# Optimization experiments

Measured on AMD Instinct MI355X. Metric: run time of the kernel, lower is better.

Reference implementation:

```python
import jax, jax.numpy as jnp
import numpy as np
from jax import lax

KS = 3
PAD = 1
N = KS * KS


def setup_inputs() -> dict:
    key = jax.random.key(0)
    k1, k2, k3, k4, k5, k6 = jax.random.split(key, 6)
    b, cin, cout, h, w = 4, 64, 64, 256, 256
    x = jax.random.normal(k1, (b, cin, h, w), jnp.float32)
    # offset-predicting conv: 2*N output channels, 3x3, pad 1
    p_conv_w = 0.1 * jax.random.normal(k2, (2 * N, cin, KS, KS), jnp.float32)
    p_conv_b = jnp.zeros((2 * N,), jnp.float32)
    # main conv applied to the k*k-expanded sampled map (no bias in original)
    conv_w = jax.random.normal(k3, (cout, cin, KS, KS), jnp.float32) / np.sqrt(cin * N)
    bn_gamma = 1.0 + 0.1 * jax.random.normal(k4, (cout,), jnp.float32)
    bn_beta = 0.1 * jax.random.normal(k5, (cout,), jnp.float32)
    return {"x": x, "p_conv_w": p_conv_w, "p_conv_b": p_conv_b,
            "conv_w": conv_w, "bn_gamma": bn_gamma, "bn_beta": bn_beta}


def _deform_conv(x, p_conv_w, p_conv_b, conv_w, bn_gamma, bn_beta):
    b, c, h, w = x.shape
    # offsets: (b, 2N, h, w) -> (b, h, w, 2N)
    offset = lax.conv_general_dilated(x, p_conv_w, (1, 1), ((PAD, PAD), (PAD, PAD)))
    offset = offset + p_conv_b[None, :, None, None]
    offset = jnp.transpose(offset, (0, 2, 3, 1))
    # zero-pad input; sampling coordinates live on the padded grid
    x_pad = jnp.pad(x, ((0, 0), (0, 0), (PAD, PAD), (PAD, PAD)))
    Hp, Wp = h + 2 * PAD, w + 2 * PAD
    # p = p_0 + p_n + offset  (x/y coords each of shape (b,h,w,N))
    r = jnp.arange(-(KS - 1) // 2, KS // 2 + 1, dtype=jnp.float32)  # [-1,0,1]
    pn_x, pn_y = jnp.meshgrid(r, r, indexing="ij")
    pn_x, pn_y = pn_x.reshape(-1), pn_y.reshape(-1)  # (N,)
    p0_x = jnp.arange(1, h + 1, dtype=jnp.float32)[:, None, None]  # (h,1,1)
    p0_y = jnp.arange(1, w + 1, dtype=jnp.float32)[None, :, None]  # (1,w,1)
    p_x = offset[..., :N] + p0_x + pn_x  # (b,h,w,N)
    p_y = offset[..., N:] + p0_y + pn_y
    # integer corner coords (detached / non-differentiable), clamped
    fx = jnp.floor(lax.stop_gradient(p_x))
    fy = jnp.floor(lax.stop_gradient(p_y))
    q_lt_x = jnp.clip(fx, 0, Hp - 1).astype(jnp.int32)
    q_lt_y = jnp.clip(fy, 0, Wp - 1).astype(jnp.int32)
    q_rb_x = jnp.clip(fx + 1, 0, Hp - 1).astype(jnp.int32)
    q_rb_y = jnp.clip(fy + 1, 0, Wp - 1).astype(jnp.int32)
    # clamped continuous coords (gradient flows to offsets)
    px = jnp.clip(p_x, 0, Hp - 1)
    py = jnp.clip(p_y, 0, Wp - 1)
    # bilinear weights
    ltx = q_lt_x.astype(px.dtype); lty = q_lt_y.astype(px.dtype)
    rbx = q_rb_x.astype(px.dtype); rby = q_rb_y.astype(px.dtype)
    g_lt = (1 + (ltx - px)) * (1 + (lty - py))
    g_rb = (1 - (rbx - px)) * (1 - (rby - py))
    g_lb = (1 + (ltx - px)) * (1 - (rby - py))
    g_rt = (1 - (rbx - px)) * (1 + (lty - py))
    x_flat = x_pad.reshape(b, c, Hp * Wp)

    def gather(qx, qy):
        idx = (qx * Wp + qy).reshape(b, 1, -1)  # (b,1,h*w*N)
        out = jnp.take_along_axis(x_flat, idx, axis=2)
        return out.reshape(b, c, h, w, N)

    x_off = (g_lt[:, None] * gather(q_lt_x, q_lt_y)
             + g_rb[:, None] * gather(q_rb_x, q_rb_y)
             + g_lb[:, None] * gather(q_lt_x, q_rb_y)
             + g_rt[:, None] * gather(q_rb_x, q_lt_y))  # (b,c,h,w,N)
    # conv (kernel=KS, stride=KS on k*k-expanded map) == contraction over (c,N)
    out = jnp.einsum("bchwn,ocn->bohw", x_off, conv_w.reshape(conv_w.shape[0], c, N))
    # BatchNorm2d (training-mode batch statistics) + LeakyReLU(0.1)
    mean = out.mean(axis=(0, 2, 3), keepdims=True)
    var = out.var(axis=(0, 2, 3), keepdims=True)
    y = (out - mean) * lax.rsqrt(var + 1e-5)
    y = y * bn_gamma[None, :, None, None] + bn_beta[None, :, None, None]
    return jnp.where(y > 0, y, 0.1 * y)


def reference(x, p_conv_w, p_conv_b, conv_w, bn_gamma, bn_beta):
    return _deform_conv(x, p_conv_w, p_conv_b, conv_w, bn_gamma, bn_beta)
```

## Files before the change

### kernel.cpp

```cpp
#include <hip/hip_runtime.h>
#include <math.h>

#define BB 4
#define CC 64
#define OCC 64
#define HH 256
#define WW 256
#define HP 258
#define WP 258
#define NPIX (BB * HH * WW)
#define CNT_F 262144.0f

typedef __attribute__((ext_vector_type(8))) __bf16 bf16x8;
typedef __attribute__((ext_vector_type(4))) float f32x4;

__global__ __launch_bounds__(256) void pad_transpose(const float* __restrict__ x,
                                                     __bf16* __restrict__ xt) {
    int blk = blockIdx.x;
    int xchunk = blk & 3;
    int y = (blk >> 2) & 255;
    int b = blk >> 10;
    int tid = threadIdx.x;
    __shared__ float tile[64][65];
    int x0 = xchunk * 64;
    int col = tid & 63;
    int crow = tid >> 6;
    const float* xp = x + ((size_t)b * CC) * HH * WW + (size_t)y * WW + x0;
#pragma unroll
    for (int i = 0; i < 16; ++i) {
        int c = crow + i * 4;
        tile[c][col] = xp[(size_t)c * HH * WW + col];
    }
    __syncthreads();
    __bf16* op = xt + (((size_t)b * HP + (y + 1)) * WP + (x0 + 1)) * CC;
#pragma unroll
    for (int i = 0; i < 16; ++i) {
        int xl = crow + i * 4;
        op[(size_t)xl * CC + col] = (__bf16)tile[col][xl];
    }
}

__global__ void zero_border(__bf16* __restrict__ xt) {
    int i = blockIdx.x * 256 + threadIdx.x;
    const int total = BB * 1028 * CC;
    if (i >= total) return;
    int c = i & 63;
    int p = (i >> 6) % 1028;
    int b = (i >> 6) / 1028;
    int yp, xp;
    if (p < 258)      { yp = 0;           xp = p; }
    else if (p < 516) { yp = 257;         xp = p - 258; }
    else if (p < 772) { yp = p - 516 + 1; xp = 0; }
    else              { yp = p - 772 + 1; xp = 257; }
    xt[(((size_t)b * HP + yp) * WP + xp) * CC + c] = (__bf16)0.0f;
}

__global__ void reorder_weights(const float* __restrict__ cw,
                                const float* __restrict__ pw,
                                __bf16* __restrict__ wtb,
                                __bf16* __restrict__ pwb) {
    int i = blockIdx.x * 256 + threadIdx.x;
    if (i < 36864) {
        int c = i & 63;
        int n = (i >> 6) % 9;
        int oc = i / 576;
        wtb[i] = (__bf16)cw[((size_t)oc * CC + c) * 9 + n];
    } else {
        int j = i - 36864;
        if (j >= 18432) return;
        int c = j & 63;
        int n = (j >> 6) % 9;
        int oc = j / 576;
        pwb[j] = (__bf16)(oc < 18 ? pw[((size_t)oc * CC + c) * 9 + n] : 0.0f);
    }
}

__global__ __launch_bounds__(256, 6) void offset_strip(const __bf16* __restrict__ xt,
                                                       const __bf16* __restrict__ pwb,
                                                       const float* __restrict__ pb,
                                                       float* __restrict__ off) {
    int phys = blockIdx.x;
    int blk = (phys & 7) * 1024 + (phys >> 3);
    int xq = blk & 7;
    int y  = (blk >> 3) & 255;
    int b  = blk >> 11;
    int x0 = xq * 32;
    int tid = threadIdx.x;
    int wave = tid >> 6, lane = tid & 63;

    __shared__ __attribute__((aligned(16))) __bf16 sS[3][34][72];
    __shared__ float sC[32][33];

    {
        const char* base = (const char*)xt + (size_t)b * HP * WP * CC * 2;
        for (int t = tid; t < 3264; t += 256) {
            int pos = t >> 5, cp = t & 31;
            int r = pos / 34, j = pos - r * 34;
            unsigned d = *(const unsigned*)(base
                + (size_t)((y + r) * WP + (x0 + j)) * (CC * 2) + cp * 4);
            *(unsigned*)&sS[r][j][cp * 2] = d;
        }
    }
    __syncthreads();

    {
        int mh = wave & 1, nh = wave >> 1;
        int m = lane & 15, q = lane >> 4;
        int p_a = mh * 16 + m;
        f32x4 acc = {0.0f, 0.0f, 0.0f, 0.0f};
        const __bf16* bp = pwb + (size_t)(nh * 16 + m) * 576 + q * 8;
#pragma unroll
        for (int n = 0; n < 9; ++n) {
            int dy = n / 3, dx = n - dy * 3;
            const __bf16* abase = &sS[dy][p_a + dx][q * 8];
#pragma unroll
            for (int h = 0; h < 2; ++h) {
                bf16x8 a  = *(const bf16x8*)(abase + h * 32);
                bf16x8 bv = *(const bf16x8*)(bp + n * 64 + h * 32);
                acc = __builtin_amdgcn_mfma_f32_16x16x32_bf16(a, bv, acc, 0, 0, 0);
            }
        }
        int oc = nh * 16 + m;
        int pxb = mh * 16 + q * 4;
#pragma unroll
        for (int r = 0; r < 4; ++r) sC[pxb + r][oc] = acc[r];
    }
    __syncthreads();

    float* ob = off + ((size_t)(b * 18)) * HH * WW + (size_t)y * WW + x0;
    for (int i = tid; i < 576; i += 256) {
        int n = i >> 5, p = i & 31;
        ob[(size_t)n * HH * WW + p] = sC[p][n] + pb[n];
    }
}

__global__ __launch_bounds__(256, 6) void deform_mfma16(const __bf16* __restrict__ xt,
                                                        const float* __restrict__ off,
                                                        const __bf16* __restrict__ wtb,
                                                        float* __restrict__ out) {
    int phys = blockIdx.x;
    int blk = (phys & 7) * 2048 + (phys >> 3);
    int xh = blk & 15;
    int y  = (blk >> 4) & 255;
    int b  = blk >> 12;
    int x0 = xh * 16;
    int tid = threadIdx.x;
    int wave = tid >> 6, lane = tid & 63;
    int chp = lane & 31, half = lane >> 5;

    __shared__ __attribute__((aligned(16))) __bf16 sA[16][584];
    __shared__ __attribute__((aligned(16))) float scratch[1152];
    float* cg = scratch;
    int*   cb = (int*)(scratch + 576);

    if (tid < 144) {
        int t = tid;
        int n = t >> 4, p = t & 15;
        float offx = off[(((size_t)(b * 18 + n)) * HH + y) * WW + x0 + p];
        float offy = off[(((size_t)(b * 18 + n + 9)) * HH + y) * WW + x0 + p];
        float px = offx + (float)(y + 1) + (float)(n / 3 - 1);
        float py = offy + (float)(x0 + p + 1) + (float)(n % 3 - 1);
        float fx = floorf(px), fy = floorf(py);
        float pxc = fminf(fmaxf(px, 0.0f), 257.0f);
        float pyc = fminf(fmaxf(py, 0.0f), 257.0f);
        int ltx = (int)fminf(fmaxf(fx, 0.0f), 257.0f);
        int lty = (int)fminf(fmaxf(fy, 0.0f), 257.0f);
        int rbx = (int)fminf(fmaxf(fx + 1.0f, 0.0f), 257.0f);
        int rby = (int)fminf(fmaxf(fy + 1.0f, 0.0f), 257.0f);
        float dxl = 1.0f + ((float)ltx - pxc);
        float dxr = 1.0f - ((float)rbx - pxc);
        float dyl = 1.0f + ((float)lty - pyc);
        float dyr = 1.0f - ((float)rby - pyc);
        cg[t * 4 + 0] = dxl * dyl;
        cg[t * 4 + 1] = dxr * dyr;
        cg[t * 4 + 2] = dxl * dyr;
        cg[t * 4 + 3] = dxr * dyl;
        cb[t * 4 + 0] = ((ltx * WP + lty) * CC) * 2;
        cb[t * 4 + 1] = ((rbx * WP + rby) * CC) * 2;
        cb[t * 4 + 2] = ((ltx * WP + rby) * CC) * 2;
        cb[t * 4 + 3] = ((rbx * WP + lty) * CC) * 2;
    }
    __syncthreads();

    {
        const char* xbl = (const char*)xt + (size_t)b * HP * WP * CC * 2 + (size_t)chp * 4;
        const float4* cg4 = (const float4*)scratch;
        const int4*   cb4 = (const int4*)(scratch + 576);
#pragma unroll 3
        for (int r = 0; r < 18; ++r) {
            int t = wave * 36 + r * 2 + half;
            float4 g = cg4[t];
            int4 cv = cb4[t];
            unsigned d0 = *(const unsigned*)(xbl + cv.x);
            unsigned d1 = *(const unsigned*)(xbl + cv.y);
            unsigned d2 = *(const unsigned*)(xbl + cv.z);
            unsigned d3 = *(const unsigned*)(xbl + cv.w);
            float lo = g.x * __builtin_bit_cast(float, d0 << 16)
                     + g.y * __builtin_bit_cast(float, d1 << 16)
                     + g.z * __builtin_bit_cast(float, d2 << 16)
                     + g.w * __builtin_bit_cast(float, d3 << 16);
            float hi = g.x * __builtin_bit_cast(float, d0 & 0xffff0000u)
                     + g.y * __builtin_bit_cast(float, d1 & 0xffff0000u)
                     + g.z * __builtin_bit_cast(float, d2 & 0xffff0000u)
                     + g.w * __builtin_bit_cast(float, d3 & 0xffff0000u);
            __bf16 rlo = (__bf16)lo, rhi = (__bf16)hi;
            ushort2 rv;
            rv.x = __builtin_bit_cast(unsigned short, rlo);
            rv.y = __builtin_bit_cast(unsigned short, rhi);
            int n = t >> 4, p = t & 15;
            *(ushort2*)&sA[p][n * 64 + chp * 2] = rv;
        }
    }
    __syncthreads();

    int m = lane & 15, q = lane >> 4;
    f32x4 acc = {0.0f, 0.0f, 0.0f, 0.0f};
    {
        const __bf16* arow = &sA[m][q * 8];
        const __bf16* bp = wtb + (size_t)(wave * 16 + m) * 576 + q * 8;
#pragma unroll
        for (int k0 = 0; k0 < 576; k0 += 32) {
            bf16x8 a  = *(const bf16x8*)(arow + k0);
            bf16x8 bv = *(const bf16x8*)(bp + k0);
            acc = __builtin_amdgcn_mfma_f32_16x16x32_bf16(a, bv, acc, 0, 0, 0);
        }
    }

    __syncthreads();
    float* sC = scratch;
    {
        int ocl = wave * 16 + m;
        int pxb = q * 4;
#pragma unroll
        for (int r = 0; r < 4; ++r)
            sC[(pxb + r) * 65 + ocl] = acc[r];
    }
    __syncthreads();
    float* ob = out + (((size_t)b * OCC) * HH + y) * WW + x0;
    for (int i = tid; i < 1024; i += 256) {
        int oc = i >> 4, p = i & 15;
        ob[(size_t)oc * HH * WW + p] = sC[p * 65 + oc];
    }
}

__global__ __launch_bounds__(256) void stats_kernel(const float* __restrict__ out,
                                                    float* __restrict__ stats) {
    int blk = blockIdx.x;
    int b = blk & 3;
    int oc = blk >> 2;
    const float* p = out + ((size_t)b * OCC + oc) * HH * WW;
    float s = 0.0f, q = 0.0f;
    for (int i = threadIdx.x; i < HH * WW; i += 256) {
        float v = p[i];
        s += v;
        q += v * v;
    }
#pragma unroll
    for (int d = 1; d < 64; d <<= 1) {
        s += __shfl_xor(s, d, 64);
        q += __shfl_xor(q, d, 64);
    }
    __shared__ float sm[8];
    int wave = threadIdx.x >> 6, lane = threadIdx.x & 63;
    if (lane == 0) { sm[wave] = s; sm[4 + wave] = q; }
    __syncthreads();
    if (threadIdx.x == 0) {
        float ts = sm[0] + sm[1] + sm[2] + sm[3];
        float tq = sm[4] + sm[5] + sm[6] + sm[7];
        atomicAdd(&stats[oc], ts);
        atomicAdd(&stats[64 + oc], tq);
    }
}

__global__ __launch_bounds__(256) void bn_leaky(float* __restrict__ out,
                                                const float* __restrict__ stats,
                                                const float* __restrict__ gamma,
                                                const float* __restrict__ beta) {
    int i = blockIdx.x * 256 + threadIdx.x;
    int oc = (i >> 14) & 63;
    float mean = stats[oc] * (1.0f / CNT_F);
    float var = stats[64 + oc] * (1.0f / CNT_F) - mean * mean;
    float scale = gamma[oc] * rsqrtf(var + 1e-5f);
    float shift = beta[oc] - mean * scale;
    float4* o4 = (float4*)out;
    float4 v = o4[i];
    v.x = v.x * scale + shift; v.x = v.x > 0.0f ? v.x : 0.1f * v.x;
    v.y = v.y * scale + shift; v.y = v.y > 0.0f ? v.y : 0.1f * v.y;
    v.z = v.z * scale + shift; v.z = v.z > 0.0f ? v.z : 0.1f * v.z;
    v.w = v.w * scale + shift; v.w = v.w > 0.0f ? v.w : 0.1f * v.w;
    o4[i] = v;
}

extern "C" void kernel_launch(void* const* d_in, const int* in_sizes, int n_in,
                              void* d_out, int out_size, void* d_ws, size_t ws_size,
                              hipStream_t stream) {
    (void)in_sizes; (void)n_in; (void)out_size; (void)ws_size;
    const float* x     = (const float*)d_in[0];
    const float* pw    = (const float*)d_in[1];
    const float* pb    = (const float*)d_in[2];
    const float* cw    = (const float*)d_in[3];
    const float* gamma = (const float*)d_in[4];
    const float* beta  = (const float*)d_in[5];
    float* out = (float*)d_out;
    char* ws = (char*)d_ws;

    __bf16* xtb  = (__bf16*)ws;
    float*  off  = (float*)(ws + 34080768);
    __bf16* wtb  = (__bf16*)(ws + 34080768 + 18874368);
    __bf16* pwb  = (__bf16*)(ws + 34080768 + 18874368 + 73728);
    float*  stats = (float*)(ws + 34080768 + 18874368 + 73728 + 36864);

    hipMemsetAsync(stats, 0, 128 * sizeof(float), stream);
    pad_transpose<<<4096, 256, 0, stream>>>(x, xtb);
    zero_border<<<(BB * 1028 * CC + 255) / 256, 256, 0, stream>>>(xtb);
    reorder_weights<<<216, 256, 0, stream>>>(cw, pw, wtb, pwb);
    offset_strip<<<8192, 256, 0, stream>>>(xtb, pwb, pb, off);
    deform_mfma16<<<16384, 256, 0, stream>>>(xtb, off, wtb, out);
    stats_kernel<<<OCC * BB, 256, 0, stream>>>(out, stats);
    bn_leaky<<<NPIX * OCC / 4 / 256, 256, 0, stream>>>(out, stats, gamma, beta);
}
```

Measured before the change: 458.0 us.

## Widen and software-pipeline deform gathers, store MFMA results directly without LDS staging

The bilinear gather in the deform kernel now has each lane load 8 bytes (4 bf16 channels) per corner instead of 4 bytes. It also prefetches the next sample's corners while the current one is blended. Each wave computes its own sampling coefficients, so one block-wide barrier goes away. Both the deform and the offset conv kernels now write MFMA accumulators straight to global memory as float4 instead of transposing through shared memory. The offset kernel's occupancy hint is raised to 8. This trades fewer barriers and LDS round trips for more registers per thread and reliance on in-wave ordering of LDS writes and reads.

```diff
diff --git a/kernel.cpp b/kernel.cpp
--- a/kernel.cpp
+++ b/kernel.cpp
@@ -13,6 +13,13 @@
 
 typedef __attribute__((ext_vector_type(8))) __bf16 bf16x8;
 typedef __attribute__((ext_vector_type(4))) float f32x4;
+
+__device__ __forceinline__ float blo(unsigned u) {
+    return __builtin_bit_cast(float, u << 16);
+}
+__device__ __forceinline__ float bhi(unsigned u) {
+    return __builtin_bit_cast(float, u & 0xffff0000u);
+}
 
 __global__ __launch_bounds__(256) void pad_transpose(const float* __restrict__ x,
                                                      __bf16* __restrict__ xt) {
@@ -75,7 +82,7 @@
     }
 }
 
-__global__ __launch_bounds__(256, 6) void offset_strip(const __bf16* __restrict__ xt,
+__global__ __launch_bounds__(256, 8) void offset_strip(const __bf16* __restrict__ xt,
                                                        const __bf16* __restrict__ pwb,
                                                        const float* __restrict__ pb,
                                                        float* __restrict__ off) {
@@ -89,7 +96,6 @@
     int wave = tid >> 6, lane = tid & 63;
 
     __shared__ __attribute__((aligned(16))) __bf16 sS[3][34][72];
-    __shared__ float sC[32][33];
 
     {
         const char* base = (const char*)xt + (size_t)b * HP * WP * CC * 2;
@@ -103,34 +109,32 @@
     }
     __syncthreads();
 
-    {
-        int mh = wave & 1, nh = wave >> 1;
-        int m = lane & 15, q = lane >> 4;
-        int p_a = mh * 16 + m;
-        f32x4 acc = {0.0f, 0.0f, 0.0f, 0.0f};
-        const __bf16* bp = pwb + (size_t)(nh * 16 + m) * 576 + q * 8;
-#pragma unroll
-        for (int n = 0; n < 9; ++n) {
-            int dy = n / 3, dx = n - dy * 3;
-            const __bf16* abase = &sS[dy][p_a + dx][q * 8];
-#pragma unroll
-            for (int h = 0; h < 2; ++h) {
-                bf16x8 a  = *(const bf16x8*)(abase + h * 32);
-                bf16x8 bv = *(const bf16x8*)(bp + n * 64 + h * 32);
-                acc = __builtin_amdgcn_mfma_f32_16x16x32_bf16(a, bv, acc, 0, 0, 0);
-            }
+    int mh = wave & 1, nh = wave >> 1;
+    int m = lane & 15, q = lane >> 4;
+    int p_a = mh * 16 + m;
+    f32x4 acc = {0.0f, 0.0f, 0.0f, 0.0f};
+    const __bf16* bp = pwb + (size_t)(nh * 16 + m) * 576 + q * 8;
+#pragma unroll
+    for (int n = 0; n < 9; ++n) {
+        int dy = n / 3, dx = n - dy * 3;
+        const __bf16* abase = &sS[dy][p_a + dx][q * 8];
+#pragma unroll
+        for (int h = 0; h < 2; ++h) {
+            bf16x8 a  = *(const bf16x8*)(abase + h * 32);
+            bf16x8 bv = *(const bf16x8*)(bp + n * 64 + h * 32);
+            acc = __builtin_amdgcn_mfma_f32_16x16x32_bf16(a, bv, acc, 0, 0, 0);
         }
-        int oc = nh * 16 + m;
-        int pxb = mh * 16 + q * 4;
-#pragma unroll
-        for (int r = 0; r < 4; ++r) sC[pxb + r][oc] = acc[r];
-    }
-    __syncthreads();
-
-    float* ob = off + ((size_t)(b * 18)) * HH * WW + (size_t)y * WW + x0;
-    for (int i = tid; i < 576; i += 256) {
-        int n = i >> 5, p = i & 31;
-        ob[(size_t)n * HH * WW + p] = sC[p][n] + pb[n];
+    }
+    int oc = nh * 16 + m;
+    if (oc < 18) {
+        float bias = pb[oc];
+        float* ob = off + (((size_t)(b * 18 + oc)) * HH + y) * WW + x0 + mh * 16 + q * 4;
+        float4 v;
+        v.x = acc[0] + bias;
+        v.y = acc[1] + bias;
+        v.z = acc[2] + bias;
+        v.w = acc[3] + bias;
+        *(float4*)ob = v;
     }
 }
 
@@ -146,15 +150,14 @@
     int x0 = xh * 16;
     int tid = threadIdx.x;
     int wave = tid >> 6, lane = tid & 63;
-    int chp = lane & 31, half = lane >> 5;
 
     __shared__ __attribute__((aligned(16))) __bf16 sA[16][584];
     __shared__ __attribute__((aligned(16))) float scratch[1152];
-    float* cg = scratch;
-    int*   cb = (int*)(scratch + 576);
-
-    if (tid < 144) {
-        int t = tid;
+    float4* cg4 = (float4*)scratch;
+    int4*   cb4 = (int4*)(scratch + 576);
+
+    if (lane < 36) {
+        int t = wave * 36 + lane;
         int n = t >> 4, p = t & 15;
         float offx = off[(((size_t)(b * 18 + n)) * HH + y) * WW + x0 + p];
         float offy = off[(((size_t)(b * 18 + n + 9)) * HH + y) * WW + x0 + p];
@@ -171,53 +174,63 @@
         float dxr = 1.0f - ((float)rbx - pxc);
         float dyl = 1.0f + ((float)lty - pyc);
         float dyr = 1.0f - ((float)rby - pyc);
-        cg[t * 4 + 0] = dxl * dyl;
-        cg[t * 4 + 1] = dxr * dyr;
-        cg[t * 4 + 2] = dxl * dyr;
-        cg[t * 4 + 3] = dxr * dyl;
-        cb[t * 4 + 0] = ((ltx * WP + lty) * CC) * 2;
-        cb[t * 4 + 1] = ((rbx * WP + rby) * CC) * 2;
-        cb[t * 4 + 2] = ((ltx * WP + rby) * CC) * 2;
-        cb[t * 4 + 3] = ((rbx * WP + lty) * CC) * 2;
+        cg4[t] = make_float4(dxl * dyl, dxr * dyr, dxl * dyr, dxr * dyl);
+        cb4[t] = make_int4(((ltx * WP + lty) * CC) * 2,
+                           ((rbx * WP + rby) * CC) * 2,
+                           ((ltx * WP + rby) * CC) * 2,
+                           ((rbx * WP + lty) * CC) * 2);
+    }
+
+    {
+        const char* xb = (const char*)xt + (size_t)b * HP * WP * CC * 2;
+        int q = lane >> 4, cl = lane & 15;
+        unsigned clb = (unsigned)cl * 8u;
+        int t = wave * 36 + q;
+        float4 g = cg4[t];
+        int4 cv = cb4[t];
+        uint2 d0 = *(const uint2*)(xb + ((unsigned)cv.x + clb));
+        uint2 d1 = *(const uint2*)(xb + ((unsigned)cv.y + clb));
+        uint2 d2 = *(const uint2*)(xb + ((unsigned)cv.z + clb));
+        uint2 d3 = *(const uint2*)(xb + ((unsigned)cv.w + clb));
+#pragma unroll
+        for (int r = 0; r < 9; ++r) {
+            float4 gn;
+            int4 cn;
+            uint2 e0, e1, e2, e3;
+            if (r < 8) {
+                int tn = t + 4;
+                gn = cg4[tn];
+                cn = cb4[tn];
+                e0 = *(const uint2*)(xb + ((unsigned)cn.x + clb));
+                e1 = *(const uint2*)(xb + ((unsigned)cn.y + clb));
+                e2 = *(const uint2*)(xb + ((unsigned)cn.z + clb));
+                e3 = *(const uint2*)(xb + ((unsigned)cn.w + clb));
+            }
+            float a0 = g.x * blo(d0.x) + g.y * blo(d1.x) + g.z * blo(d2.x) + g.w * blo(d3.x);
+            float a1 = g.x * bhi(d0.x) + g.y * bhi(d1.x) + g.z * bhi(d2.x) + g.w * bhi(d3.x);
+            float a2 = g.x * blo(d0.y) + g.y * blo(d1.y) + g.z * blo(d2.y) + g.w * blo(d3.y);
+            float a3 = g.x * bhi(d0.y) + g.y * bhi(d1.y) + g.z * bhi(d2.y) + g.w * bhi(d3.y);
+            ushort4 rv;
+            rv.x = __builtin_bit_cast(unsigned short, (__bf16)a0);
+            rv.y = __builtin_bit_cast(unsigned short, (__bf16)a1);
+            rv.z = __builtin_bit_cast(unsigned short, (__bf16)a2);
+            rv.w = __builtin_bit_cast(unsigned short, (__bf16)a3);
+            int n = t >> 4, p = t & 15;
+            *(ushort4*)&sA[p][n * 64 + cl * 4] = rv;
+            if (r < 8) {
+                t += 4;
+                g = gn; cv = cn;
+                d0 = e0; d1 = e1; d2 = e2; d3 = e3;
+            }
+        }
     }
     __syncthreads();
 
-    {
-        const char* xbl = (const char*)xt + (size_t)b * HP * WP * CC * 2 + (size_t)chp * 4;
-        const float4* cg4 = (const float4*)scratch;
-        const int4*   cb4 = (const int4*)(scratch + 576);
-#pragma unroll 3
-        for (int r = 0; r < 18; ++r) {
-            int t = wave * 36 + r * 2 + half;
-            float4 g = cg4[t];
-            int4 cv = cb4[t];
-            unsigned d0 = *(const unsigned*)(xbl + cv.x);
-            unsigned d1 = *(const unsigned*)(xbl + cv.y);
-            unsigned d2 = *(const unsigned*)(xbl + cv.z);
-            unsigned d3 = *(const unsigned*)(xbl + cv.w);
-            float lo = g.x * __builtin_bit_cast(float, d0 << 16)
-                     + g.y * __builtin_bit_cast(float, d1 << 16)
-                     + g.z * __builtin_bit_cast(float, d2 << 16)
-                     + g.w * __builtin_bit_cast(float, d3 << 16);
-            float hi = g.x * __builtin_bit_cast(float, d0 & 0xffff0000u)
-                     + g.y * __builtin_bit_cast(float, d1 & 0xffff0000u)
-                     + g.z * __builtin_bit_cast(float, d2 & 0xffff0000u)
-                     + g.w * __builtin_bit_cast(float, d3 & 0xffff0000u);
-            __bf16 rlo = (__bf16)lo, rhi = (__bf16)hi;
-            ushort2 rv;
-            rv.x = __builtin_bit_cast(unsigned short, rlo);
-            rv.y = __builtin_bit_cast(unsigned short, rhi);
-            int n = t >> 4, p = t & 15;
-            *(ushort2*)&sA[p][n * 64 + chp * 2] = rv;
-        }
-    }
-    __syncthreads();
-
-    int m = lane & 15, q = lane >> 4;
+    int m = lane & 15, q2 = lane >> 4;
     f32x4 acc = {0.0f, 0.0f, 0.0f, 0.0f};
     {
-        const __bf16* arow = &sA[m][q * 8];
-        const __bf16* bp = wtb + (size_t)(wave * 16 + m) * 576 + q * 8;
+        const __bf16* arow = &sA[m][q2 * 8];
+        const __bf16* bp = wtb + (size_t)(wave * 16 + m) * 576 + q2 * 8;
 #pragma unroll
         for (int k0 = 0; k0 < 576; k0 += 32) {
             bf16x8 a  = *(const bf16x8*)(arow + k0);
@@ -226,21 +239,9 @@
         }
     }
 
-    __syncthreads();
-    float* sC = scratch;
-    {
-        int ocl = wave * 16 + m;
-        int pxb = q * 4;
-#pragma unroll
-        for (int r = 0; r < 4; ++r)
-            sC[(pxb + r) * 65 + ocl] = acc[r];
-    }
-    __syncthreads();
-    float* ob = out + (((size_t)b * OCC) * HH + y) * WW + x0;
-    for (int i = tid; i < 1024; i += 256) {
-        int oc = i >> 4, p = i & 15;
-        ob[(size_t)oc * HH * WW + p] = sC[p * 65 + oc];
-    }
+    int oc = wave * 16 + m;
+    float* ob = out + (((size_t)b * OCC + oc) * HH + y) * WW + x0 + q2 * 4;
+    *(f32x4*)ob = acc;
 }
 
 __global__ __launch_bounds__(256) void stats_kernel(const float* __restrict__ out,
```

After: 478.1 us. 4.4% more time.
